# Kernel tuning notes

Measured on AMD Instinct MI355X. Metric: run time of the kernel, lower is better.

Reference implementation:

```python
import jax, jax.numpy as jnp
import numpy as np

FEATURE_MAPS = (38, 19, 10, 5, 3, 1)
BOXES_PER_LOC = (4, 6, 6, 6, 4, 4)
IMAGE_SIZE = 300
DEC_SIZE = 64  # WhatDecoder output resolution
MAX_OBJECTS = 10
Z_WHAT = 64


def _recon_indices():
    # Maps per-prior slots (8732) to per-location slots (1940), matching
    # Decoder.reconstruction_indices: each location index repeated boxes_per_loc times.
    idx, last = [], 0
    for fm, bpl in zip(FEATURE_MAPS, BOXES_PER_LOC):
        loc = np.arange(fm * fm) + last
        idx.append(np.repeat(loc, bpl))
        last = loc[-1] + 1
    return jnp.asarray(np.concatenate(idx), dtype=jnp.int32)


def _deconv2x2(x, W, b):
    # ConvTranspose2d(kernel=2, stride=2): each input pixel expands to a 2x2 block.
    n, c, h, w = x.shape
    o = W.shape[1]
    y = jnp.einsum('nchw,coab->nohawb', x, W).reshape(n, o, 2 * h, 2 * w)
    return y + b[None, :, None, None]


def _what_decoder(z, params):
    # z (M, Z_WHAT) -> (M, 3, 64, 64) in [0,1]
    x = z[:, :, None, None]
    nl = len(params)
    for i, (W, b) in enumerate(params):
        x = _deconv2x2(x, W, b)
        x = jax.nn.relu(x) if i < nl - 1 else jax.nn.sigmoid(x)
    return x


def _stn(images, z_where):
    # Spatial transformer: place (M,3,S,S) glyphs into IMAGE_SIZE canvas at box
    # z_where (M,4) = (cx,cy,w,h) in [0,1]; bilinear sampling, zeros padding.
    M, _, S, _ = images.shape
    cx, cy, w, h = (z_where[:, i] for i in range(4))
    # output pixel centers in normalized [-1,1] coords (align_corners=False)
    coords = (2.0 * jnp.arange(IMAGE_SIZE, dtype=images.dtype) + 1.0) / IMAGE_SIZE - 1.0
    xo = coords[None, None, :]
    yo = coords[None, :, None]
    eps = 1e-6
    u = (xo - (2.0 * cx - 1.0)[:, None, None]) / (w[:, None, None] + eps)  # (M,H,W)
    v = (yo - (2.0 * cy - 1.0)[:, None, None]) / (h[:, None, None] + eps)
    ix = ((u + 1.0) * S - 1.0) / 2.0  # input pixel coords
    iy = ((v + 1.0) * S - 1.0) / 2.0

    def sample_one(img, iy, ix):
        iy0 = jnp.floor(iy)
        ix0 = jnp.floor(ix)
        wy1 = iy - iy0
        wx1 = ix - ix0
        wy0 = 1.0 - wy1
        wx0 = 1.0 - wx1

        def g(y, x):
            yi = jnp.clip(y, 0, S - 1).astype(jnp.int32)
            xi = jnp.clip(x, 0, S - 1).astype(jnp.int32)
            valid = ((y >= 0) & (y < S) & (x >= 0) & (x < S)).astype(img.dtype)
            return img[:, yi, xi] * valid  # (3,H,W)

        return (g(iy0, ix0) * wy0 * wx0 + g(iy0, ix0 + 1) * wy0 * wx1
                + g(iy0 + 1, ix0) * wy1 * wx0 + g(iy0 + 1, ix0 + 1) * wy1 * wx1)

    return jax.vmap(sample_one)(images, iy, ix)  # (M,3,H,H)


def setup_inputs() -> dict:
    key = jax.random.key(0)
    ks = jax.random.split(key, 20)
    B, NLOC, NPRI = 16, 1940, 8732
    chans = (Z_WHAT, 256, 128, 64, 32, 16, 3)
    inp = {
        'z_what': jax.random.normal(ks[0], (B, NLOC, Z_WHAT), jnp.float32),
        'z_where': jax.random.uniform(ks[1], (B, NPRI, 4), jnp.float32),
        'z_present': jax.random.randint(ks[2], (B, NPRI, 1), 0, 2, jnp.int32),
        'z_depth': jax.random.normal(ks[3], (B, NLOC, 1), jnp.float32),
    }
    for i in range(6):
        ci, co = chans[i], chans[i + 1]
        inp[f'W{i}'] = jax.random.normal(ks[4 + i], (ci, co, 2, 2), jnp.float32) * 0.1
        inp[f'b{i}'] = jnp.zeros((co,), jnp.float32)
    return inp


def reference(z_what, z_where, z_present, z_depth,
              W0, b0, W1, b1, W2, b2, W3, b3, W4, b4, W5, b5):
    params = [(W0, b0), (W1, b1), (W2, b2), (W3, b3), (W4, b4), (W5, b5)]
    idx = _recon_indices()
    zw = z_what[:, idx]      # (B, P, D) ragged location->prior gather
    zd = z_depth[:, idx, 0]  # (B, P)
    order = jnp.argsort(-zd, axis=1)[:, :MAX_OBJECTS]  # depth sort, descending
    B, K = order.shape

    def gat(t):
        return jnp.take_along_axis(
            t, jnp.broadcast_to(order[:, :, None], (B, K, t.shape[-1])), axis=1)

    sw = gat(zw)            # (B,K,D)
    swr = gat(z_where)      # (B,K,4)
    sp = gat(z_present)     # (B,K,1)

    decoded = _what_decoder(sw.reshape(B * K, Z_WHAT), params)      # (B*K,3,64,64)
    transformed = _stn(decoded, swr.reshape(B * K, 4))              # (B*K,3,300,300)
    present = (sp == 1).astype(transformed.dtype).reshape(B * K, 1, 1, 1)
    objs = (transformed * present).reshape(B, K, 3, IMAGE_SIZE, IMAGE_SIZE)

    # z-buffer merge: per pixel, take first nonzero object in depth order
    nz = objs != 0.0
    first = nz & (jnp.cumsum(nz.astype(jnp.int32), axis=1) == 1)
    return jnp.sum(objs * first.astype(objs.dtype), axis=1)  # (B,3,300,300)
```

## Files before the change

kernel.cpp:

```cpp
#include <hip/hip_runtime.h>
#include <cmath>

#define NLOC 1940
#define NPRI 8732
#define BATCH 16
#define KOBJ 10

__device__ __forceinline__ void ins3(float v, int i,
    float& a0, float& a1, float& a2, int& j0, int& j1, int& j2)
{
    if (v > a0 || (v == a0 && i < j0)) { a2=a1; j2=j1; a1=a0; j1=j0; a0=v; j0=i; }
    else if (v > a1 || (v == a1 && i < j1)) { a2=a1; j2=j1; a1=v; j1=i; }
    else if (v > a2 || (v == a2 && i < j2)) { a2=v; j2=i; }
}

__device__ __forceinline__ float ix_chain(int x, float shift, float wh) {
    const float xo = __fsub_rn(__fdiv_rn(__fadd_rn(__fmul_rn(2.0f, (float)x), 1.0f), 300.0f), 1.0f);
    const float u  = __fdiv_rn(__fsub_rn(xo, shift), wh);
    return __fmul_rn(__fsub_rn(__fmul_rn(__fadd_rn(u, 1.0f), 64.0f), 1.0f), 0.5f);
}

__global__ __launch_bounds__(256) void prep_kernel(
    const float* __restrict__ W0, const float* __restrict__ W1, float* __restrict__ Wr,
    const float* __restrict__ z_what, const float* __restrict__ z_where,
    const int* __restrict__ z_present, const float* __restrict__ z_depth,
    float* __restrict__ gathered, float* __restrict__ paramsF, int* __restrict__ paramsI,
    int* __restrict__ obnd)
{
    __shared__ float sv[768];
    __shared__ int   si[768];
    __shared__ int   locs3[3];
    __shared__ int   sj_start[3], sj_bpl[3];
    __shared__ int   spres[10], sjj[10];
    __shared__ float szw[10][4];
    __shared__ float lpf[KOBJ][4];
    __shared__ int   lcnt;
    const int tid = threadIdx.x;

    if (blockIdx.x < 768) {
        const int idx = blockIdx.x * 256 + tid;
        if (idx < 65536) {
            int q = idx >> 14, rem = idx & 16383, c = rem >> 8, o = rem & 255;
            Wr[idx] = W0[(((c << 8) | o) << 2) + q];
        } else {
            int i2 = idx - 65536;
            int q = i2 >> 15, rem = i2 & 32767, c = rem >> 7, o = rem & 127;
            Wr[idx] = W1[(((c << 7) | o) << 2) + q];
        }
        return;
    }

    const int b = blockIdx.x - 768;
    float v0 = -INFINITY, v1 = -INFINITY, v2 = -INFINITY;
    int   i0 = NLOC, i1 = NLOC, i2 = NLOC;
    for (int i = tid; i < NLOC; i += 256) {
        float v = z_depth[b * NLOC + i];
        ins3(v, i, v0, v1, v2, i0, i1, i2);
    }
    sv[tid*3+0] = v0; sv[tid*3+1] = v1; sv[tid*3+2] = v2;
    si[tid*3+0] = i0; si[tid*3+1] = i1; si[tid*3+2] = i2;
    __syncthreads();
    for (int s = 128; s > 0; s >>= 1) {
        if (tid < s) {
            float a0 = sv[tid*3], a1 = sv[tid*3+1], a2 = sv[tid*3+2];
            int   j0 = si[tid*3], j1 = si[tid*3+1], j2 = si[tid*3+2];
            const int o = tid + s;
            ins3(sv[o*3+0], si[o*3+0], a0, a1, a2, j0, j1, j2);
            ins3(sv[o*3+1], si[o*3+1], a0, a1, a2, j0, j1, j2);
            ins3(sv[o*3+2], si[o*3+2], a0, a1, a2, j0, j1, j2);
            sv[tid*3] = a0; sv[tid*3+1] = a1; sv[tid*3+2] = a2;
            si[tid*3] = j0; si[tid*3+1] = j1; si[tid*3+2] = j2;
        }
        __syncthreads();
    }

    if (tid < 3) {
        int L = si[tid];
        locs3[tid] = L;
        int start, bpl;
        if (L < 1444)      { start = 4 * L;                 bpl = 4; }
        else if (L < 1805) { start = 5776 + 6 * (L - 1444); bpl = 6; }
        else if (L < 1905) { start = 7942 + 6 * (L - 1805); bpl = 6; }
        else if (L < 1930) { start = 8542 + 6 * (L - 1905); bpl = 6; }
        else if (L < 1939) { start = 8692 + 4 * (L - 1930); bpl = 4; }
        else               { start = 8728;                  bpl = 4; }
        sj_start[tid] = start; sj_bpl[tid] = bpl;
    }
    __syncthreads();
    if (tid < 10) {
        const int b0 = sj_bpl[0], b1 = sj_bpl[1];
        int j, o;
        if (tid < b0)           { j = 0; o = tid; }
        else if (tid < b0 + b1) { j = 1; o = tid - b0; }
        else                    { j = 2; o = tid - b0 - b1; }
        const int p = sj_start[j] + o;
        sjj[tid]   = j;
        spres[tid] = z_present[b * NPRI + p];
        const float4 zw = *reinterpret_cast<const float4*>(z_where + (b * NPRI + p) * 4);
        szw[tid][0] = zw.x; szw[tid][1] = zw.y; szw[tid][2] = zw.z; szw[tid][3] = zw.w;
    }
    __syncthreads();
    if (tid == 0) {
        int cnt = 0;
        for (int i = 0; i < 10; ++i) {
            if (spres[i] == 1) {
                float p0 = __fadd_rn(szw[i][2], 1e-6f);
                float p1 = __fadd_rn(szw[i][3], 1e-6f);
                float p2 = __fsub_rn(__fmul_rn(2.0f, szw[i][0]), 1.0f);
                float p3 = __fsub_rn(__fmul_rn(2.0f, szw[i][1]), 1.0f);
                float* pf = paramsF + (b * KOBJ + cnt) * 4;
                pf[0] = p0; pf[1] = p1; pf[2] = p2; pf[3] = p3;
                lpf[cnt][0] = p0; lpf[cnt][1] = p1; lpf[cnt][2] = p2; lpf[cnt][3] = p3;
                paramsI[b * 12 + 2 + cnt] = b * 3 + sjj[i];
                cnt++;
            }
        }
        paramsI[b * 12] = cnt;
        lcnt = cnt;
    }
    __syncthreads();
    if (tid < 4 * KOBJ) {
        const int k = tid >> 2, ty = tid & 3;
        if (k < lcnt) {
            const float wh = (ty < 2) ? lpf[k][0] : lpf[k][1];
            const float sh = (ty < 2) ? lpf[k][2] : lpf[k][3];
            int res;
            if ((ty & 1) == 0) {
                int lo = 0, hi = 300;
                while (lo < hi) { int m = (lo + hi) >> 1;
                    if (ix_chain(m, sh, wh) > -1.0f) hi = m; else lo = m + 1; }
                res = lo;
            } else {
                int lo = -1, hi = 299;
                while (lo < hi) { int m = (lo + hi + 1) >> 1;
                    if (ix_chain(m, sh, wh) < 64.0f) lo = m; else hi = m - 1; }
                res = lo;
            }
            obnd[(b * KOBJ + k) * 4 + ty] = res;
        }
    }
    if (tid < 192) {
        int j = tid >> 6, c = tid & 63;
        gathered[(b * 3 + j) * 64 + c] = z_what[(b * NLOC + locs3[j]) * 64 + c];
    }
}

__global__ __launch_bounds__(256) void dec_fused(
    const float* __restrict__ gathered, const float* __restrict__ Wr,
    const float* __restrict__ b0v, const float* __restrict__ b1v,
    const float* __restrict__ W2, const float* __restrict__ b2v,
    const float* __restrict__ W3, const float* __restrict__ b3v,
    const float* __restrict__ W4, const float* __restrict__ b4v,
    const float* __restrict__ W5, const float* __restrict__ b5v,
    float* __restrict__ decoded)
{
    __shared__ __align__(16) float P[2048];
    __shared__ __align__(16) float Q[1024];
    __shared__ __align__(16) float Zs[128];
    const int r  = blockIdx.x;
    const int g  = blockIdx.y;
    const int t  = threadIdx.x;
    const int y1 = r >> 2, x1 = r & 3;
    const int q0 = (y1 >> 1) * 2 + (x1 >> 1);
    const int p1 = (y1 & 1) * 2 + (x1 & 1);
    const int s2 = g * 2;

    if (t < 128) Zs[t] = gathered[(s2 + (t & 1)) * 64 + (t >> 1)];
    __syncthreads();

    {
        const float* w0 = Wr + q0 * 16384 + t;
        float bv = b0v[t];
        float2 acc = make_float2(bv, bv);
        #pragma unroll 8
        for (int c = 0; c < 64; ++c) {
            float w = w0[c << 8];
            float2 xs = *reinterpret_cast<const float2*>(Zs + (c << 1));
            acc.x = fmaf(xs.x, w, acc.x); acc.y = fmaf(xs.y, w, acc.y);
        }
        *reinterpret_cast<float2*>(P + (t << 1)) =
            make_float2(fmaxf(acc.x, 0.f), fmaxf(acc.y, 0.f));
    }
    __syncthreads();

    {
        const int o = t & 127, h = t >> 7;
        const float* w1 = Wr + 65536 + p1 * 32768 + o;
        float2 acc;
        if (h == 0) { float bv = b1v[o]; acc = make_float2(bv, bv); }
        else        { acc = make_float2(0.f, 0.f); }
        const int cb = h << 7;
        #pragma unroll 8
        for (int c = 0; c < 128; ++c) {
            float w = w1[(cb + c) << 7];
            float2 xs = *reinterpret_cast<const float2*>(P + ((cb + c) << 1));
            acc.x = fmaf(xs.x, w, acc.x); acc.y = fmaf(xs.y, w, acc.y);
        }
        if (h == 1) *reinterpret_cast<float2*>(P + 512 + (o << 1)) = acc;
        __syncthreads();
        if (h == 0) {
            float2 p2 = *reinterpret_cast<const float2*>(P + 512 + (o << 1));
            acc.x += p2.x; acc.y += p2.y;
            *reinterpret_cast<float2*>(Q + (o << 1)) =
                make_float2(fmaxf(acc.x, 0.f), fmaxf(acc.y, 0.f));
        }
    }
    __syncthreads();

    {
        const float* w2 = W2 + t;
        float bv = b2v[t >> 2];
        float2 acc = make_float2(bv, bv);
        #pragma unroll 8
        for (int ci = 0; ci < 128; ++ci) {
            float w = w2[ci << 8];
            float2 xs = *reinterpret_cast<const float2*>(Q + (ci << 1));
            acc.x = fmaf(xs.x, w, acc.x); acc.y = fmaf(xs.y, w, acc.y);
        }
        *reinterpret_cast<float2*>(P + (t << 1)) =
            make_float2(fmaxf(acc.x, 0.f), fmaxf(acc.y, 0.f));
    }
    __syncthreads();

    {
        const int px = t & 15, coa = t >> 4;
        const int ly = px >> 2, lx = px & 3;
        const int par = (ly >> 1) * 2 + (lx >> 1);
        const int wp  = (ly & 1) * 2 + (lx & 1);
        const float* w3 = W3 + coa * 4 + wp;
        float bva = b3v[coa], bvb = b3v[coa + 16];
        float2 a0 = make_float2(bva, bva);
        float2 a1 = make_float2(bvb, bvb);
        #pragma unroll 8
        for (int ci = 0; ci < 64; ++ci) {
            float2 xs = *reinterpret_cast<const float2*>(P + (ci << 3) + (par << 1));
            float wa = w3[ci << 7];
            float wb = w3[(ci << 7) + 64];
            a0.x = fmaf(xs.x, wa, a0.x); a0.y = fmaf(xs.y, wa, a0.y);
            a1.x = fmaf(xs.x, wb, a1.x); a1.y = fmaf(xs.y, wb, a1.y);
        }
        *reinterpret_cast<float2*>(Q + (coa << 5) + (px << 1)) =
            make_float2(fmaxf(a0.x, 0.f), fmaxf(a0.y, 0.f));
        *reinterpret_cast<float2*>(Q + ((coa + 16) << 5) + (px << 1)) =
            make_float2(fmaxf(a1.x, 0.f), fmaxf(a1.y, 0.f));
    }
    __syncthreads();

    {
        const int px = t & 63, co0 = t >> 6;
        const int ly = px >> 3, lx = px & 7;
        const int par = (ly >> 1) * 4 + (lx >> 1);
        const int wp  = (ly & 1) * 2 + (lx & 1);
        const float* w4 = W4 + co0 * 4 + wp;
        float2 acc[4];
        #pragma unroll
        for (int k = 0; k < 4; ++k) { float bv = b4v[co0 + 4 * k]; acc[k] = make_float2(bv, bv); }
        #pragma unroll 4
        for (int ci = 0; ci < 32; ++ci) {
            float2 xs = *reinterpret_cast<const float2*>(Q + (ci << 5) + (par << 1));
            #pragma unroll
            for (int k = 0; k < 4; ++k) {
                float w = w4[(ci << 6) + k * 16];
                acc[k].x = fmaf(xs.x, w, acc[k].x); acc[k].y = fmaf(xs.y, w, acc[k].y);
            }
        }
        #pragma unroll
        for (int k = 0; k < 4; ++k)
            *reinterpret_cast<float2*>(P + ((co0 + 4 * k) << 7) + (px << 1)) =
                make_float2(fmaxf(acc[k].x, 0.f), fmaxf(acc[k].y, 0.f));
    }
    __syncthreads();

    {
        const int px = t;
        const int ly = px >> 4, lx = px & 15;
        const int par = (ly >> 1) * 8 + (lx >> 1);
        const int wp  = (ly & 1) * 2 + (lx & 1);
        const int gy = y1 * 16 + ly, gx = x1 * 16 + lx;
        const float* w5 = W5 + wp;
        float2 acc[3];
        #pragma unroll
        for (int c = 0; c < 3; ++c) { float bv = b5v[c]; acc[c] = make_float2(bv, bv); }
        #pragma unroll 4
        for (int ci = 0; ci < 16; ++ci) {
            float2 xs = *reinterpret_cast<const float2*>(P + (ci << 7) + (par << 1));
            #pragma unroll
            for (int c = 0; c < 3; ++c) {
                float w = w5[ci * 12 + c * 4];
                acc[c].x = fmaf(xs.x, w, acc[c].x); acc[c].y = fmaf(xs.y, w, acc[c].y);
            }
        }
        const int pbase = (gy * 64 + gx) * 3;
        #pragma unroll
        for (int c = 0; c < 3; ++c) {
            decoded[(s2 + 0) * 12288 + pbase + c] = 1.0f / (1.0f + expf(-acc[c].x));
            decoded[(s2 + 1) * 12288 + pbase + c] = 1.0f / (1.0f + expf(-acc[c].y));
        }
    }
}

__global__ __launch_bounds__(256) void stn_kernel(
    const float* __restrict__ decoded, const float* __restrict__ paramsF,
    const int* __restrict__ paramsI, const int* __restrict__ obnd,
    float* __restrict__ out)
{
    const int b = blockIdx.y;
    const int pix0 = blockIdx.x * 256;
    const int yfirst = pix0 / 300;
    __shared__ float sp[KOBJ][4];
    __shared__ int   ssamp[KOBJ];
    __shared__ int   s_xlo[KOBJ], s_xhi[KOBJ], s_ylo[KOBJ], s_yhi[KOBJ];
    __shared__ int   scnt;
    __shared__ float s_wy0[KOBJ][2], s_wy1[KOBJ][2];
    __shared__ int   s_rb0[KOBJ][2], s_rb1[KOBJ][2];
    __shared__ unsigned char s_cov[KOBJ][2];
    __shared__ unsigned char s_vy[KOBJ][2];
    __shared__ int s_list[KOBJ];
    __shared__ int s_lc;
    const int tid = threadIdx.x;

    if (tid == 0) scnt = paramsI[b * 12];
    if (tid < KOBJ) {
        #pragma unroll
        for (int c = 0; c < 4; ++c) sp[tid][c] = paramsF[(b * KOBJ + tid) * 4 + c];
        ssamp[tid] = paramsI[b * 12 + 2 + tid];
        const int4 bd = *reinterpret_cast<const int4*>(obnd + (b * KOBJ + tid) * 4);
        s_xlo[tid] = bd.x; s_xhi[tid] = bd.y; s_ylo[tid] = bd.z; s_yhi[tid] = bd.w;
    }
    __syncthreads();

    if (tid < 2 * scnt) {
        const int k = tid >> 1, sel = tid & 1;
        int yy = yfirst + sel; if (yy > 299) yy = 299;
        const bool cov = (yy >= s_ylo[k]) && (yy <= s_yhi[k]);
        s_cov[k][sel] = cov ? 1 : 0;
        if (cov) {
            const float iy = ix_chain(yy, sp[k][3], sp[k][1]);
            const float iy0f = floorf(iy);
            const float iy1f = __fadd_rn(iy0f, 1.0f);
            const float wy1  = __fsub_rn(iy, iy0f);
            s_wy1[k][sel] = wy1;
            s_wy0[k][sel] = __fsub_rn(1.0f, wy1);
            const bool vy0 = (iy0f >= 0.0f) && (iy0f < 64.0f);
            const bool vy1 = (iy1f >= 0.0f) && (iy1f < 64.0f);
            s_vy[k][sel] = (unsigned char)((vy0 ? 1 : 0) | (vy1 ? 2 : 0));
            s_rb0[k][sel] = ((int)fminf(fmaxf(iy0f, 0.0f), 63.0f)) * 64;
            s_rb1[k][sel] = ((int)fminf(fmaxf(iy1f, 0.0f), 63.0f)) * 64;
        }
    }
    __syncthreads();
    if (tid == 0) {
        int lc = 0;
        for (int k = 0; k < scnt; ++k)
            if (s_cov[k][0] | s_cov[k][1]) s_list[lc++] = k;
        s_lc = lc;
    }
    __syncthreads();

    const int pix = pix0 + tid;
    if (pix < 90000) {
        const int y = pix / 300;
        const int x = pix - y * 300;
        const int rs = y - yfirst;
        float o0 = 0.0f, o1 = 0.0f, o2 = 0.0f;
        bool d0 = false, d1 = false, d2 = false;
        const int lc = s_lc;
        for (int m = 0; m < lc; ++m) {
            const int k = s_list[m];
            if (!s_cov[k][rs]) continue;
            if (x < s_xlo[k] || x > s_xhi[k]) continue;

            const float ix = ix_chain(x, sp[k][2], sp[k][0]);
            const float ix0f = floorf(ix);
            const float ix1f = __fadd_rn(ix0f, 1.0f);
            const float wx1 = __fsub_rn(ix, ix0f);
            const float wx0 = __fsub_rn(1.0f, wx1);
            const bool vx0 = (ix0f >= 0.0f) && (ix0f < 64.0f);
            const bool vx1 = (ix1f >= 0.0f) && (ix1f < 64.0f);
            const int x0 = (int)fminf(fmaxf(ix0f, 0.0f), 63.0f);
            const int x1 = (int)fminf(fmaxf(ix1f, 0.0f), 63.0f);

            const float wy0 = s_wy0[k][rs], wy1 = s_wy1[k][rs];
            const int rb0 = s_rb0[k][rs], rb1 = s_rb1[k][rs];
            const unsigned char vy = s_vy[k][rs];
            const bool m00 = (vy & 1) && vx0, m01 = (vy & 1) && vx1;
            const bool m10 = (vy & 2) && vx0, m11 = (vy & 2) && vx1;
            const float* img = decoded + ssamp[k] * 12288;

            float g00x = 0.f, g00y = 0.f, g00z = 0.f;
            float g01x = 0.f, g01y = 0.f, g01z = 0.f;
            float g10x = 0.f, g10y = 0.f, g10z = 0.f;
            float g11x = 0.f, g11y = 0.f, g11z = 0.f;
            if (m00) { const float* p = img + (rb0 + x0) * 3; g00x = p[0]; g00y = p[1]; g00z = p[2]; }
            if (m01) { const float* p = img + (rb0 + x1) * 3; g01x = p[0]; g01y = p[1]; g01z = p[2]; }
            if (m10) { const float* p = img + (rb1 + x0) * 3; g10x = p[0]; g10y = p[1]; g10z = p[2]; }
            if (m11) { const float* p = img + (rb1 + x1) * 3; g11x = p[0]; g11y = p[1]; g11z = p[2]; }

            if (!d0) {
                float val = g00x * wy0 * wx0 + g01x * wy0 * wx1 + g10x * wy1 * wx0 + g11x * wy1 * wx1;
                if (val != 0.0f) { o0 = val; d0 = true; }
            }
            if (!d1) {
                float val = g00y * wy0 * wx0 + g01y * wy0 * wx1 + g10y * wy1 * wx0 + g11y * wy1 * wx1;
                if (val != 0.0f) { o1 = val; d1 = true; }
            }
            if (!d2) {
                float val = g00z * wy0 * wx0 + g01z * wy0 * wx1 + g10z * wy1 * wx0 + g11z * wy1 * wx1;
                if (val != 0.0f) { o2 = val; d2 = true; }
            }
            if (d0 && d1 && d2) break;
        }
        const int ob = b * 270000 + pix;
        out[ob] = o0;
        out[ob + 90000] = o1;
        out[ob + 180000] = o2;
    }
}

extern "C" void kernel_launch(void* const* d_in, const int* in_sizes, int n_in,
                              void* d_out, int out_size, void* d_ws, size_t ws_size,
                              hipStream_t stream)
{
    const float* z_what    = (const float*)d_in[0];
    const float* z_where   = (const float*)d_in[1];
    const int*   z_present = (const int*)d_in[2];
    const float* z_depth   = (const float*)d_in[3];
    const float* W0 = (const float*)d_in[4];   const float* b0 = (const float*)d_in[5];
    const float* W1 = (const float*)d_in[6];   const float* b1 = (const float*)d_in[7];
    const float* W2 = (const float*)d_in[8];   const float* b2 = (const float*)d_in[9];
    const float* W3 = (const float*)d_in[10];  const float* b3 = (const float*)d_in[11];
    const float* W4 = (const float*)d_in[12];  const float* b4 = (const float*)d_in[13];
    const float* W5 = (const float*)d_in[14];  const float* b5 = (const float*)d_in[15];

    float* ws = (float*)d_ws;
    float* gathered = ws;
    float* paramsF  = ws + 16384;
    int*   paramsI  = (int*)(ws + 17408);
    int*   obnd     = (int*)(ws + 17664);
    float* decoded  = ws + 32768;
    float* Wr       = (float*)d_out;
    float* outp     = (float*)d_out;

    hipLaunchKernelGGL(prep_kernel, dim3(784), dim3(256), 0, stream,
                       W0, W1, Wr, z_what, z_where, z_present, z_depth,
                       gathered, paramsF, paramsI, obnd);
    hipLaunchKernelGGL(dec_fused, dim3(16, 24), dim3(256), 0, stream,
                       gathered, Wr, b0, b1, W2, b2, W3, b3, W4, b4, W5, b5, decoded);
    hipLaunchKernelGGL(stn_kernel, dim3(352, BATCH), dim3(256), 0, stream,
                       decoded, paramsF, paramsI, obnd, outp);
}
```

Baseline: 150.1 us.

## Decode one sample per block and pad decoded glyphs to float4 RGBA

The decoder kernel now processes one sample per block instead of two, doubling the grid to use more CUs but halving weight reuse per load. The decoded image layout is padded from 3 to 4 channels, so the decoder writes one float4 per pixel and the STN kernel gathers each bilinear tap with a single 16-byte load instead of three scalar loads. This costs more workspace memory traffic for the padded channel.

```diff
diff --git a/kernel.cpp b/kernel.cpp
--- a/kernel.cpp
+++ b/kernel.cpp
@@ -154,71 +154,51 @@
     const float* __restrict__ W5, const float* __restrict__ b5v,
     float* __restrict__ decoded)
 {
-    __shared__ __align__(16) float P[2048];
-    __shared__ __align__(16) float Q[1024];
-    __shared__ __align__(16) float Zs[128];
+    __shared__ __align__(16) float P[1024];
+    __shared__ __align__(16) float Q[512];
+    __shared__ __align__(16) float Zs[64];
     const int r  = blockIdx.x;
-    const int g  = blockIdx.y;
+    const int s  = blockIdx.y;
     const int t  = threadIdx.x;
     const int y1 = r >> 2, x1 = r & 3;
     const int q0 = (y1 >> 1) * 2 + (x1 >> 1);
     const int p1 = (y1 & 1) * 2 + (x1 & 1);
-    const int s2 = g * 2;
-
-    if (t < 128) Zs[t] = gathered[(s2 + (t & 1)) * 64 + (t >> 1)];
+
+    if (t < 64) Zs[t] = gathered[s * 64 + t];
     __syncthreads();
 
     {
         const float* w0 = Wr + q0 * 16384 + t;
-        float bv = b0v[t];
-        float2 acc = make_float2(bv, bv);
+        float acc = b0v[t];
         #pragma unroll 8
-        for (int c = 0; c < 64; ++c) {
-            float w = w0[c << 8];
-            float2 xs = *reinterpret_cast<const float2*>(Zs + (c << 1));
-            acc.x = fmaf(xs.x, w, acc.x); acc.y = fmaf(xs.y, w, acc.y);
-        }
-        *reinterpret_cast<float2*>(P + (t << 1)) =
-            make_float2(fmaxf(acc.x, 0.f), fmaxf(acc.y, 0.f));
+        for (int c = 0; c < 64; ++c)
+            acc = fmaf(Zs[c], w0[c << 8], acc);
+        P[t] = fmaxf(acc, 0.f);
     }
     __syncthreads();
 
     {
         const int o = t & 127, h = t >> 7;
         const float* w1 = Wr + 65536 + p1 * 32768 + o;
-        float2 acc;
-        if (h == 0) { float bv = b1v[o]; acc = make_float2(bv, bv); }
-        else        { acc = make_float2(0.f, 0.f); }
+        float acc = (h == 0) ? b1v[o] : 0.f;
         const int cb = h << 7;
         #pragma unroll 8
-        for (int c = 0; c < 128; ++c) {
-            float w = w1[(cb + c) << 7];
-            float2 xs = *reinterpret_cast<const float2*>(P + ((cb + c) << 1));
-            acc.x = fmaf(xs.x, w, acc.x); acc.y = fmaf(xs.y, w, acc.y);
-        }
-        if (h == 1) *reinterpret_cast<float2*>(P + 512 + (o << 1)) = acc;
+        for (int c = 0; c < 128; ++c)
+            acc = fmaf(P[cb + c], w1[(cb + c) << 7], acc);
+        if (h == 1) P[256 + o] = acc;
         __syncthreads();
-        if (h == 0) {
-            float2 p2 = *reinterpret_cast<const float2*>(P + 512 + (o << 1));
-            acc.x += p2.x; acc.y += p2.y;
-            *reinterpret_cast<float2*>(Q + (o << 1)) =
-                make_float2(fmaxf(acc.x, 0.f), fmaxf(acc.y, 0.f));
-        }
+        if (h == 0)
+            Q[o] = fmaxf(acc + P[256 + o], 0.f);
     }
     __syncthreads();
 
     {
         const float* w2 = W2 + t;
-        float bv = b2v[t >> 2];
-        float2 acc = make_float2(bv, bv);
+        float acc = b2v[t >> 2];
         #pragma unroll 8
-        for (int ci = 0; ci < 128; ++ci) {
-            float w = w2[ci << 8];
-            float2 xs = *reinterpret_cast<const float2*>(Q + (ci << 1));
-            acc.x = fmaf(xs.x, w, acc.x); acc.y = fmaf(xs.y, w, acc.y);
-        }
-        *reinterpret_cast<float2*>(P + (t << 1)) =
-            make_float2(fmaxf(acc.x, 0.f), fmaxf(acc.y, 0.f));
+        for (int ci = 0; ci < 128; ++ci)
+            acc = fmaf(Q[ci], w2[ci << 8], acc);
+        P[t] = fmaxf(acc, 0.f);
     }
     __syncthreads();
 
@@ -228,21 +208,16 @@
         const int par = (ly >> 1) * 2 + (lx >> 1);
         const int wp  = (ly & 1) * 2 + (lx & 1);
         const float* w3 = W3 + coa * 4 + wp;
-        float bva = b3v[coa], bvb = b3v[coa + 16];
-        float2 a0 = make_float2(bva, bva);
-        float2 a1 = make_float2(bvb, bvb);
+        float a0 = b3v[coa];
+        float a1 = b3v[coa + 16];
         #pragma unroll 8
         for (int ci = 0; ci < 64; ++ci) {
-            float2 xs = *reinterpret_cast<const float2*>(P + (ci << 3) + (par << 1));
-            float wa = w3[ci << 7];
-            float wb = w3[(ci << 7) + 64];
-            a0.x = fmaf(xs.x, wa, a0.x); a0.y = fmaf(xs.y, wa, a0.y);
-            a1.x = fmaf(xs.x, wb, a1.x); a1.y = fmaf(xs.y, wb, a1.y);
-        }
-        *reinterpret_cast<float2*>(Q + (coa << 5) + (px << 1)) =
-            make_float2(fmaxf(a0.x, 0.f), fmaxf(a0.y, 0.f));
-        *reinterpret_cast<float2*>(Q + ((coa + 16) << 5) + (px << 1)) =
-            make_float2(fmaxf(a1.x, 0.f), fmaxf(a1.y, 0.f));
+            float xs = P[(ci << 2) + par];
+            a0 = fmaf(xs, w3[ci << 7], a0);
+            a1 = fmaf(xs, w3[(ci << 7) + 64], a1);
+        }
+        Q[(coa << 4) + px] = fmaxf(a0, 0.f);
+        Q[((coa + 16) << 4) + px] = fmaxf(a1, 0.f);
     }
     __syncthreads();
 
@@ -252,22 +227,19 @@
         const int par = (ly >> 1) * 4 + (lx >> 1);
         const int wp  = (ly & 1) * 2 + (lx & 1);
         const float* w4 = W4 + co0 * 4 + wp;
-        float2 acc[4];
+        float acc[4];
         #pragma unroll
-        for (int k = 0; k < 4; ++k) { float bv = b4v[co0 + 4 * k]; acc[k] = make_float2(bv, bv); }
+        for (int k = 0; k < 4; ++k) acc[k] = b4v[co0 + 4 * k];
         #pragma unroll 4
         for (int ci = 0; ci < 32; ++ci) {
-            float2 xs = *reinterpret_cast<const float2*>(Q + (ci << 5) + (par << 1));
+            float xs = Q[(ci << 4) + par];
             #pragma unroll
-            for (int k = 0; k < 4; ++k) {
-                float w = w4[(ci << 6) + k * 16];
-                acc[k].x = fmaf(xs.x, w, acc[k].x); acc[k].y = fmaf(xs.y, w, acc[k].y);
-            }
+            for (int k = 0; k < 4; ++k)
+                acc[k] = fmaf(xs, w4[(ci << 6) + k * 16], acc[k]);
         }
         #pragma unroll
         for (int k = 0; k < 4; ++k)
-            *reinterpret_cast<float2*>(P + ((co0 + 4 * k) << 7) + (px << 1)) =
-                make_float2(fmaxf(acc[k].x, 0.f), fmaxf(acc[k].y, 0.f));
+            P[((co0 + 4 * k) << 6) + px] = fmaxf(acc[k], 0.f);
     }
     __syncthreads();
 
@@ -278,24 +250,23 @@
         const int wp  = (ly & 1) * 2 + (lx & 1);
         const int gy = y1 * 16 + ly, gx = x1 * 16 + lx;
         const float* w5 = W5 + wp;
-        float2 acc[3];
+        float acc[3];
         #pragma unroll
-        for (int c = 0; c < 3; ++c) { float bv = b5v[c]; acc[c] = make_float2(bv, bv); }
+        for (int c = 0; c < 3; ++c) acc[c] = b5v[c];
         #pragma unroll 4
         for (int ci = 0; ci < 16; ++ci) {
-            float2 xs = *reinterpret_cast<const float2*>(P + (ci << 7) + (par << 1));
+            float xs = P[(ci << 6) + par];
             #pragma unroll
-            for (int c = 0; c < 3; ++c) {
-                float w = w5[ci * 12 + c * 4];
-                acc[c].x = fmaf(xs.x, w, acc[c].x); acc[c].y = fmaf(xs.y, w, acc[c].y);
-            }
-        }
-        const int pbase = (gy * 64 + gx) * 3;
-        #pragma unroll
-        for (int c = 0; c < 3; ++c) {
-            decoded[(s2 + 0) * 12288 + pbase + c] = 1.0f / (1.0f + expf(-acc[c].x));
-            decoded[(s2 + 1) * 12288 + pbase + c] = 1.0f / (1.0f + expf(-acc[c].y));
-        }
+            for (int c = 0; c < 3; ++c)
+                acc[c] = fmaf(xs, w5[ci * 12 + c * 4], acc[c]);
+        }
+        const int pbase = (gy * 64 + gx) * 4;
+        float4 v;
+        v.x = 1.0f / (1.0f + expf(-acc[0]));
+        v.y = 1.0f / (1.0f + expf(-acc[1]));
+        v.z = 1.0f / (1.0f + expf(-acc[2]));
+        v.w = 0.0f;
+        *reinterpret_cast<float4*>(decoded + s * 16384 + pbase) = v;
     }
 }
 
@@ -385,27 +356,24 @@
             const unsigned char vy = s_vy[k][rs];
             const bool m00 = (vy & 1) && vx0, m01 = (vy & 1) && vx1;
             const bool m10 = (vy & 2) && vx0, m11 = (vy & 2) && vx1;
-            const float* img = decoded + ssamp[k] * 12288;
-
-            float g00x = 0.f, g00y = 0.f, g00z = 0.f;
-            float g01x = 0.f, g01y = 0.f, g01z = 0.f;
-            float g10x = 0.f, g10y = 0.f, g10z = 0.f;
-            float g11x = 0.f, g11y = 0.f, g11z = 0.f;
-            if (m00) { const float* p = img + (rb0 + x0) * 3; g00x = p[0]; g00y = p[1]; g00z = p[2]; }
-            if (m01) { const float* p = img + (rb0 + x1) * 3; g01x = p[0]; g01y = p[1]; g01z = p[2]; }
-            if (m10) { const float* p = img + (rb1 + x0) * 3; g10x = p[0]; g10y = p[1]; g10z = p[2]; }
-            if (m11) { const float* p = img + (rb1 + x1) * 3; g11x = p[0]; g11y = p[1]; g11z = p[2]; }
+            const float* img = decoded + ssamp[k] * 16384;
+
+            const float4 z4 = make_float4(0.f, 0.f, 0.f, 0.f);
+            const float4 g00 = m00 ? *reinterpret_cast<const float4*>(img + ((rb0 + x0) << 2)) : z4;
+            const float4 g01 = m01 ? *reinterpret_cast<const float4*>(img + ((rb0 + x1) << 2)) : z4;
+            const float4 g10 = m10 ? *reinterpret_cast<const float4*>(img + ((rb1 + x0) << 2)) : z4;
+            const float4 g11 = m11 ? *reinterpret_cast<const float4*>(img + ((rb1 + x1) << 2)) : z4;
 
             if (!d0) {
-                float val = g00x * wy0 * wx0 + g01x * wy0 * wx1 + g10x * wy1 * wx0 + g11x * wy1 * wx1;
+                float val = g00.x * wy0 * wx0 + g01.x * wy0 * wx1 + g10.x * wy1 * wx0 + g11.x * wy1 * wx1;
                 if (val != 0.0f) { o0 = val; d0 = true; }
             }
             if (!d1) {
-                float val = g00y * wy0 * wx0 + g01y * wy0 * wx1 + g10y * wy1 * wx0 + g11y * wy1 * wx1;
+                float val = g00.y * wy0 * wx0 + g01.y * wy0 * wx1 + g10.y * wy1 * wx0 + g11.y * wy1 * wx1;
                 if (val != 0.0f) { o1 = val; d1 = true; }
             }
             if (!d2) {
-                float val = g00z * wy0 * wx0 + g01z * wy0 * wx1 + g10z * wy1 * wx0 + g11z * wy1 * wx1;
+                float val = g00.z * wy0 * wx0 + g01.z * wy0 * wx1 + g10.z * wy1 * wx0 + g11.z * wy1 * wx1;
                 if (val != 0.0f) { o2 = val; d2 = true; }
             }
             if (d0 && d1 && d2) break;
@@ -444,7 +412,7 @@
     hipLaunchKernelGGL(prep_kernel, dim3(784), dim3(256), 0, stream,
                        W0, W1, Wr, z_what, z_where, z_present, z_depth,
                        gathered, paramsF, paramsI, obnd);
-    hipLaunchKernelGGL(dec_fused, dim3(16, 24), dim3(256), 0, stream,
+    hipLaunchKernelGGL(dec_fused, dim3(16, 48), dim3(256), 0, stream,
                        gathered, Wr, b0, b1, W2, b2, W3, b3, W4, b4, W5, b5, decoded);
     hipLaunchKernelGGL(stn_kernel, dim3(352, BATCH), dim3(256), 0, stream,
                        decoded, paramsF, paramsI, obnd, outp);
```

Result: slower. 153.2 us (+2.1%).
